# Performance work log

Measured on AMD Instinct MI355X. Metric: run time of the kernel, lower is better.

Reference implementation:

```python
import jax, jax.numpy as jnp
import numpy as np
from jax import lax

K = 9  # propagation kernel

def conv(x, w, b, pad):
    y = lax.conv_general_dilated(x, w, (1, 1), [(pad, pad), (pad, pad)],
                                 dimension_numbers=('NCHW', 'OIHW', 'NCHW'))
    return y + b[None, :, None, None]

def bn(x, g, beta):
    # SynchronizedBatchNorm2d in eval mode with identity running stats (mean=0, var=1)
    return x * g[None, :, None, None] + beta[None, :, None, None]

def propagate(deep, wts):
    # Dynamic local filtering (same math as img2col * weights, sum over 81 taps),
    # computed as 81 shifted-slice FMAs instead of materializing the (n,c,hw,81) tensor.
    p = K // 2
    n, c, h, w = deep.shape
    padded = jnp.pad(deep, ((0, 0), (0, 0), (p, p), (p, p)))
    out = jnp.zeros_like(deep)
    for k in range(K * K):  # k = dy*9 + dx, matching unfold(2).unfold(3) flattening
        dy, dx = k // K, k % K
        out = out + padded[:, :, dy:dy + h, dx:dx + w] * wts[:, k:k + 1]
    return out

def setup_inputs():
    key = jax.random.key(0)
    ks = jax.random.split(key, 40)
    N, C, H, W = 1, 256, 96, 192
    NUM_CLASSES = 19
    s = 0.05
    f32 = jnp.float32
    d = {}
    d['f1_deep'] = jax.random.normal(ks[0], (N, C, H, W), f32)
    d['f1_low'] = jax.random.normal(ks[1], (N, C, H, W), f32)
    d['f2_low'] = jax.random.normal(ks[2], (N, C, H, W), f32)
    # WeightPredictor
    d['wp_c1_w'] = jax.random.normal(ks[3], (256, 256, 3, 3), f32) * s
    d['wp_c1_b'] = jnp.zeros((256,), f32)
    d['wp_c2_w'] = jax.random.normal(ks[4], (256, 512, 3, 3), f32) * s
    d['wp_c2_b'] = jnp.zeros((256,), f32)
    d['wp_fc_w'] = jax.random.normal(ks[5], (81, 256, 1, 1), f32) * s
    d['wp_fc_b'] = jnp.zeros((81,), f32)
    # AdaptiveScheduler
    d['sch_c1_w'] = jax.random.normal(ks[6], (256, 256, 3, 3), f32) * s
    d['sch_c1_b'] = jnp.zeros((256,), f32)
    d['sch_c2_w'] = jax.random.normal(ks[7], (256, 256, 3, 3), f32) * s
    d['sch_c2_b'] = jnp.zeros((256,), f32)
    d['sch_fc_w'] = jax.random.normal(ks[8], (1, 256), f32) * s
    d['sch_fc_b'] = jnp.zeros((1,), f32)
    # AdaptNet
    d['ad_c1_w'] = jax.random.normal(ks[9], (256, 512, 3, 3), f32) * s
    d['ad_c1_b'] = jnp.zeros((256,), f32)
    d['ad_c2_w'] = jax.random.normal(ks[10], (256, 256, 3, 3), f32) * s
    d['ad_c2_b'] = jnp.zeros((256,), f32)
    d['ad_c3_w'] = jax.random.normal(ks[11], (256, 256, 3, 3), f32) * s
    d['ad_c3_b'] = jnp.zeros((256,), f32)
    # reduce_conv2 (1x1 conv + BN)
    d['rc_w'] = jax.random.normal(ks[12], (48, 256, 1, 1), f32) * s
    d['rc_b'] = jnp.zeros((48,), f32)
    d['rc_g'] = jnp.ones((48,), f32)
    d['rc_beta'] = jnp.zeros((48,), f32)
    # last_conv
    d['lc1_w'] = jax.random.normal(ks[13], (256, 304, 3, 3), f32) * s
    d['lc1_b'] = jnp.zeros((256,), f32)
    d['lc1_g'] = jnp.ones((256,), f32)
    d['lc1_beta'] = jnp.zeros((256,), f32)
    d['lc2_w'] = jax.random.normal(ks[14], (256, 256, 3, 3), f32) * s
    d['lc2_b'] = jnp.zeros((256,), f32)
    d['lc2_g'] = jnp.ones((256,), f32)
    d['lc2_beta'] = jnp.zeros((256,), f32)
    d['lc3_w'] = jax.random.normal(ks[15], (NUM_CLASSES, 256, 1, 1), f32) * s
    d['lc3_b'] = jnp.zeros((NUM_CLASSES,), f32)
    return d

def reference(f1_deep, f1_low, f2_low,
              wp_c1_w, wp_c1_b, wp_c2_w, wp_c2_b, wp_fc_w, wp_fc_b,
              sch_c1_w, sch_c1_b, sch_c2_w, sch_c2_b, sch_fc_w, sch_fc_b,
              ad_c1_w, ad_c1_b, ad_c2_w, ad_c2_b, ad_c3_w, ad_c3_b,
              rc_w, rc_b, rc_g, rc_beta,
              lc1_w, lc1_b, lc1_g, lc1_beta,
              lc2_w, lc2_b, lc2_g, lc2_beta,
              lc3_w, lc3_b):
    n, c, h, w = f1_deep.shape
    # WeightPredictor: shared conv1 applied to both low features, cat, conv2, 1x1, softmax over 81 taps
    a1 = conv(f1_low, wp_c1_w, wp_c1_b, 1)
    a2 = conv(f2_low, wp_c1_w, wp_c1_b, 1)
    f = conv(jnp.concatenate([a1, a2], axis=1), wp_c2_w, wp_c2_b, 1)
    kernel = jax.nn.softmax(conv(f, wp_fc_w, wp_fc_b, 0), axis=1)  # (n,81,h,w)
    # AdaptiveScheduler
    diff = conv(f1_low, sch_c1_w, sch_c1_b, 1) - conv(f2_low, sch_c1_w, sch_c1_b, 1)
    o = conv(diff, sch_c2_w, sch_c2_b, 1)
    pooled = jnp.mean(o, axis=(2, 3)).squeeze()  # (256,) since n=1
    deviation = pooled @ sch_fc_w.T + sch_fc_b  # (1,)
    # PropagationModule (dynamic 9x9 local filtering of f1_deep by predicted per-pixel kernel)
    prop = propagate(f1_deep, kernel)  # (n,256,h,w)
    # AdaptNet
    x = conv(jnp.concatenate([f2_low, prop], axis=1), ad_c1_w, ad_c1_b, 1)
    x = conv(x, ad_c2_w, ad_c2_b, 1)
    x = conv(x, ad_c3_w, ad_c3_b, 1)
    # reduce_conv2 + last_conv
    low = bn(conv(f2_low, rc_w, rc_b, 0), rc_g, rc_beta)  # (n,48,h,w)
    x = jnp.concatenate([x, low], axis=1)  # (n,304,h,w)
    x = bn(conv(x, lc1_w, lc1_b, 1), lc1_g, lc1_beta)
    x = bn(conv(x, lc2_w, lc2_b, 1), lc2_g, lc2_beta)
    x = conv(x, lc3_w, lc3_b, 0)  # (n,19,h,w)
    out = jax.image.resize(x, (x.shape[0], x.shape[1], 4 * h, 4 * w), method='bilinear')
    return (out, deviation)
```

## Files before the change

kernel.cpp:

```cpp
#include <hip/hip_runtime.h>
#include <math.h>

#define HWIMG 18432
#define W2 194
#define H2 98
#define NPX1 (H2 * W2)
#define W4 200
#define H4 104
#define NPX4 (H4 * W4)
#define NOUT (19 * 384 * 768)

typedef short bf16x8 __attribute__((ext_vector_type(8)));
typedef float f32x16 __attribute__((ext_vector_type(16)));

__device__ __forceinline__ ushort bf16r(float f) {
    union { float f; unsigned u; } a; a.f = f;
    unsigned u = a.u;
    return (ushort)((u + 0x7fffu + ((u >> 16) & 1u)) >> 16);
}
__device__ __forceinline__ float b2f(ushort u) {
    union { unsigned i; float f; } a; a.i = ((unsigned)u) << 16;
    return a.f;
}
__device__ __forceinline__ bf16x8 ld8(const ushort* p) {
    return *reinterpret_cast<const bf16x8*>(p);
}

__device__ __forceinline__ void gld16(const ushort* g, ushort* l) {
    __builtin_amdgcn_global_load_lds(
        (const __attribute__((address_space(1))) unsigned int*)g,
        (__attribute__((address_space(3))) unsigned int*)l, 16, 0, 0);
}

#define MF32(a, b, c) __builtin_amdgcn_mfma_f32_32x32x16_bf16(a, b, c, 0, 0, 0)


__global__ __launch_bounds__(256) void xform_t_k(const float* __restrict__ src,
                                                 const float* __restrict__ src2,
                                                 ushort* __restrict__ dst)
{
    const int px = blockIdx.x * 32 + (threadIdx.x & 31);
    const int c8 = (blockIdx.y * 8 + (threadIdx.x >> 5)) * 8;
    if (px >= NPX1) return;
    const int yP = px / W2, xP = px % W2;
    const int y = yP - 1, x = xP - 1;
    ushort v[8];
    if (y >= 0 && y < 96 && x >= 0 && x < 192) {
        const int p = y * 192 + x;
#pragma unroll
        for (int j = 0; j < 8; ++j) {
            float f = src[(size_t)(c8 + j) * HWIMG + p];
            if (src2) f -= src2[(size_t)(c8 + j) * HWIMG + p];
            v[j] = bf16r(f);
        }
    } else {
#pragma unroll
        for (int j = 0; j < 8; ++j) v[j] = 0;
    }
    *reinterpret_cast<uint4*>(dst + ((size_t)(c8 >> 4) * NPX1 + px) * 16 + (c8 & 15))
        = *reinterpret_cast<uint4*>(v);
}

__global__ __launch_bounds__(256) void xform_nhwc_k(const float* __restrict__ src,
                                                    ushort* __restrict__ dst)
{
    const int px = blockIdx.x * 8 + (threadIdx.x >> 5);
    const int c8 = (threadIdx.x & 31) * 8;
    if (px >= NPX4) return;
    const int yP = px / W4, xP = px % W4;
    const int y = yP - 4, x = xP - 4;
    ushort v[8];
    if (y >= 0 && y < 96 && x >= 0 && x < 192) {
        const int p = y * 192 + x;
#pragma unroll
        for (int j = 0; j < 8; ++j) v[j] = bf16r(src[(size_t)(c8 + j) * HWIMG + p]);
    } else {
#pragma unroll
        for (int j = 0; j < 8; ++j) v[j] = 0;
    }
    *reinterpret_cast<uint4*>(dst + (size_t)px * 256 + c8) = *reinterpret_cast<uint4*>(v);
}

__global__ __launch_bounds__(256) void borderzero3_k(ushort* __restrict__ b0,
                                                     ushort* __restrict__ b1,
                                                     ushort* __restrict__ b2)
{
    ushort* buf = (blockIdx.y == 0) ? b0 : ((blockIdx.y == 1) ? b1 : b2);
    const int idx = blockIdx.x * 256 + threadIdx.x;
    if (idx >= 580 * 16) return;
    const int pi = idx % 580;
    const int cb = idx / 580;
    int pp;
    if (pi < 194) pp = pi;
    else if (pi < 388) pp = 97 * 194 + (pi - 194);
    else if (pi < 484) pp = (pi - 388 + 1) * 194;
    else pp = (pi - 484 + 1) * 194 + 193;
    uint4 z = {0, 0, 0, 0};
    ushort* p = buf + ((size_t)cb * NPX1 + pp) * 16;
    *reinterpret_cast<uint4*>(p) = z;
    *reinterpret_cast<uint4*>(p + 8) = z;
}

struct WtxJob {
    const float* w; const float* b; const float* g; const float* beta;
    int CoutR, Coutp, CinR0, kb0e, CinR1, KBt, ntaps, wtoff, biasoff;
};

__global__ __launch_bounds__(256) void wtx_multi_k(WtxJob J0, WtxJob J1, WtxJob J2,
                                                   WtxJob J3, WtxJob J4, WtxJob J5,
                                                   ushort* __restrict__ wt,
                                                   float* __restrict__ biasout)
{
    WtxJob J = J0;
    switch (blockIdx.y) {
        case 1: J = J1; break; case 2: J = J2; break; case 3: J = J3; break;
        case 4: J = J4; break; case 5: J = J5; break; default: break;
    }
    const int idx = blockIdx.x * 256 + threadIdx.x;
    const int total = J.ntaps * J.KBt * J.Coutp * 16;
    const int CinT = J.CinR0 + J.CinR1;
    if (idx < total) {
        const int c16 = idx & 15;
        const int oc = (idx >> 4) % J.Coutp;
        const int r2 = idx / (16 * J.Coutp);
        const int tap = r2 % J.ntaps;
        const int kbt = r2 / J.ntaps;
        const int k = kbt * 16 + c16;
        float val = 0.f;
        if (oc < J.CoutR) {
            int cit = -1;
            if (k < J.kb0e) { if (k < J.CinR0) cit = k; }
            else { const int k1 = k - J.kb0e; if (k1 < J.CinR1) cit = J.CinR0 + k1; }
            if (cit >= 0) {
                val = J.w[((size_t)oc * CinT + cit) * J.ntaps + tap];
                if (J.g) val *= J.g[oc];
            }
        }
        wt[J.wtoff + idx] = bf16r(val);
    } else if (idx < total + J.Coutp) {
        const int oc = idx - total;
        float v = 0.f;
        if (oc < J.CoutR) {
            v = J.b ? J.b[oc] : 0.f;
            if (J.g) v = v * J.g[oc] + J.beta[oc];
        }
        biasout[J.biasoff + oc] = v;
    }
}

struct ConvJob {
    const ushort* in0; const ushort* in1;
    int KB0, KB1;
    const ushort* wt;
    const float* bias;
    ushort* out;
    int CoutWr;
};

template<int NTAPS>
__device__ __forceinline__ void stage_kb(
    const ConvJob& J, int kb, char* Ab, char* Bb,
    int y0, int x0, int ocb0, int Coutp, int tid)
{
    constexpr int AROWS = (NTAPS == 9) ? 4 : 2;
    constexpr int AW = (NTAPS == 9) ? 66 : 64;
    constexpr int ASLOTS = AROWS * AW * 2;
    const ushort* plane = (kb < J.KB0)
        ? (J.in0 + (size_t)kb * (NPX1 * 16))
        : (J.in1 + (size_t)(kb - J.KB0) * (NPX1 * 16));
#pragma unroll
    for (int i = 0; i < (ASLOTS + 127) / 128; ++i) {
        const int f16 = i * 128 + tid;
        if ((ASLOTS % 128 == 0) || (f16 < ASLOTS)) {
            const int e = f16 >> 1;
            const int h8 = (f16 & 1) * 8;
            const int r = e / AW;
            const int xx = e - r * AW;
            const int px = (NTAPS == 9)
                ? (y0 - 1 + r) * W2 + (x0 - 1 + xx)
                : (y0 + r) * W2 + (x0 + xx);
            gld16(plane + (size_t)px * 16 + h8,
                  (ushort*)(Ab + __builtin_amdgcn_readfirstlane((f16 & ~63) * 16)));
        }
    }
    const ushort* wsrc = J.wt + ((size_t)(kb * NTAPS) * Coutp + ocb0 + (tid >> 1)) * 16
                       + (tid & 1) * 8;
    const int wu = __builtin_amdgcn_readfirstlane((tid & ~63) * 16);
#pragma unroll
    for (int t = 0; t < NTAPS; ++t) {
        gld16(wsrc + (size_t)t * Coutp * 16, (ushort*)(Bb + t * 2048 + wu));
    }
}

template<int NTAPS>
__device__ __forceinline__ void compute_step(
    f32x16& c00, f32x16& c01, f32x16& c10, f32x16& c11,
    const char* Ab, const char* Bb, int wm, int l31, int h16)
{
    constexpr int AW = (NTAPS == 9) ? 66 : 64;
#pragma unroll
    for (int t = 0; t < NTAPS; ++t) {
        const int rowb = (NTAPS == 9) ? ((wm + t / 3) * AW + (t % 3)) : (wm * AW);
        const char* Bp = Bb + t * 2048;
        bf16x8 a0 = ld8((const ushort*)(Ab + (rowb + l31) * 32 + h16));
        bf16x8 a1 = ld8((const ushort*)(Ab + (rowb + 32 + l31) * 32 + h16));
        bf16x8 b0 = ld8((const ushort*)(Bp + l31 * 32 + h16));
        bf16x8 b1 = ld8((const ushort*)(Bp + (32 + l31) * 32 + h16));
        c00 = MF32(a0, b0, c00);
        c01 = MF32(a0, b1, c01);
        c10 = MF32(a1, b0, c10);
        c11 = MF32(a1, b1, c11);
    }
}

template<int NTAPS>
__global__ __launch_bounds__(128) void conv_lds_k(ConvJob j0, ConvJob j1, ConvJob j2,
                                                  int Coutp)
{
    constexpr int AROWS = (NTAPS == 9) ? 4 : 2;
    constexpr int AW = (NTAPS == 9) ? 66 : 64;
    constexpr int APLANE = AROWS * AW * 32;
    __shared__ __align__(128) char A0[APLANE];
    __shared__ __align__(128) char A1[APLANE];
    __shared__ __align__(128) char B0[NTAPS * 2048];
    __shared__ __align__(128) char B1[NTAPS * 2048];

    ConvJob J = j0;
    if (blockIdx.y == 1) J = j1;
    else if (blockIdx.y == 2) J = j2;

    const int nblk = gridDim.x;
    const int cpx = nblk >> 3;
    const int sw = ((int)blockIdx.x & 7) * cpx + ((int)blockIdx.x >> 3);
    const int pt = sw % 144;
    const int ocb0 = (sw / 144) * 64;
    const int y0 = (pt / 3) * 2 + 1;
    const int x0 = (pt % 3) * 64 + 1;

    const int tid = threadIdx.x;
    const int lane = tid & 63;
    const int wm = tid >> 6;
    const int l31 = lane & 31;
    const int h16 = (lane >> 5) * 16;

    const int KBtot = J.KB0 + J.KB1;

    f32x16 c00 = {}, c01 = {}, c10 = {}, c11 = {};

    stage_kb<NTAPS>(J, 0, A0, B0, y0, x0, ocb0, Coutp, tid);
    __syncthreads();

    for (int s = 0; s < KBtot; s += 2) {
        stage_kb<NTAPS>(J, s + 1, A1, B1, y0, x0, ocb0, Coutp, tid);
        __builtin_amdgcn_sched_barrier(0);
        compute_step<NTAPS>(c00, c01, c10, c11, A0, B0, wm, l31, h16);
        __syncthreads();
        if (s + 2 < KBtot)
            stage_kb<NTAPS>(J, s + 2, A0, B0, y0, x0, ocb0, Coutp, tid);
        __builtin_amdgcn_sched_barrier(0);
        compute_step<NTAPS>(c00, c01, c10, c11, A1, B1, wm, l31, h16);
        __syncthreads();
    }

    const int pxbase = (y0 + wm) * W2 + x0;
    const int rlo = (lane >> 5) * 4;
#pragma unroll
    for (int j = 0; j < 2; ++j) {
        if (ocb0 + j * 32 + 32 > J.CoutWr) continue;
        const int oc = ocb0 + j * 32 + l31;
        const float bs = J.bias[oc];
        const size_t obase = (size_t)(oc >> 4) * ((size_t)NPX1 * 16) + (oc & 15);
        const f32x16 v0 = j ? c01 : c00;
        const f32x16 v1 = j ? c11 : c10;
#pragma unroll
        for (int r = 0; r < 16; ++r) {
            const int rw = (r & 3) + 8 * (r >> 2) + rlo;
            J.out[obase + (size_t)(pxbase + rw) * 16] = bf16r(v0[r] + bs);
            J.out[obase + (size_t)(pxbase + 32 + rw) * 16] = bf16r(v1[r] + bs);
        }
    }
}

__global__ __launch_bounds__(256) void softmax81_k(ushort* __restrict__ t)
{
    const int p = blockIdx.x * 256 + threadIdx.x;
    if (p >= HWIMG) return;
    const int y = p / 192, x = p % 192;
    const size_t pp = (size_t)(y + 1) * W2 + (x + 1);
    float v[81];
    float m = -1e30f;
#pragma unroll
    for (int k = 0; k < 81; ++k) {
        v[k] = b2f(t[((size_t)(k >> 4) * NPX1 + pp) * 16 + (k & 15)]);
        m = fmaxf(m, v[k]);
    }
    float s = 0.f;
#pragma unroll
    for (int k = 0; k < 81; ++k) { v[k] = __expf(v[k] - m); s += v[k]; }
    const float inv = 1.f / s;
#pragma unroll
    for (int k = 0; k < 81; ++k)
        t[((size_t)(k >> 4) * NPX1 + pp) * 16 + (k & 15)] = bf16r(v[k] * inv);
}

__global__ __launch_bounds__(256) void prop_k(const ushort* __restrict__ deep,
                                              const ushort* __restrict__ ker,
                                              ushort* __restrict__ out)
{
    __shared__ float kl[8][81];
    const int pxb = blockIdx.x * 8;
    const int t = threadIdx.x;
    for (int i = t; i < 8 * 81; i += 256) {
        const int pp = pxb + i / 81, k = i % 81;
        float kv = 0.f;
        if (pp < NPX1) {
            const int yP = pp / W2, xP = pp % W2;
            if (yP >= 1 && yP <= 96 && xP >= 1 && xP <= 192)
                kv = b2f(ker[((size_t)(k >> 4) * NPX1 + pp) * 16 + (k & 15)]);
        }
        kl[i / 81][k] = kv;
    }
    __syncthreads();
    const int pi = t >> 5;
    const int c8 = (t & 31) * 8;
    const int pp = pxb + pi;
    if (pp >= NPX1) return;
    const int yP = pp / W2, xP = pp % W2;
    ushort* op = out + ((size_t)(c8 >> 4) * NPX1 + pp) * 16 + (c8 & 15);
    if (yP < 1 || yP > 96 || xP < 1 || xP > 192) {
        uint4 z = {0, 0, 0, 0};
        *reinterpret_cast<uint4*>(op) = z;
        return;
    }
    const int y = yP - 1, x = xP - 1;
    float acc[8];
#pragma unroll
    for (int j = 0; j < 8; ++j) acc[j] = 0.f;
    const ushort* dbase = deep + ((size_t)(y + 4) * W4 + (x + 4)) * 256 + c8;
#pragma unroll
    for (int k = 0; k < 81; ++k) {
        const int dy = k / 9 - 4, dx = k % 9 - 4;
        const float kv = kl[pi][k];
        bf16x8 d = ld8(dbase + (ptrdiff_t)(dy * W4 + dx) * 256);
#pragma unroll
        for (int j = 0; j < 8; ++j) acc[j] += b2f((ushort)d[j]) * kv;
    }
    ushort v[8];
#pragma unroll
    for (int j = 0; j < 8; ++j) v[j] = bf16r(acc[j]);
    *reinterpret_cast<uint4*>(op) = *reinterpret_cast<uint4*>(v);
}

__global__ __launch_bounds__(256) void rowsum_k(const ushort* __restrict__ t,
                                                float* __restrict__ partial)
{
    const int y = blockIdx.x >> 2;
    const int bx = blockIdx.x & 3;
    const int c = threadIdx.x;
    const size_t base = ((size_t)(c >> 4) * NPX1 + (size_t)(y + 1) * W2 + 1 + bx * 48) * 16
                      + (c & 15);
    float s = 0.f;
    for (int x = 0; x < 48; ++x) s += b2f(t[base + (size_t)x * 16]);
    partial[(size_t)blockIdx.x * 256 + c] = s;
}

__global__ __launch_bounds__(256) void dev_k(const float* __restrict__ partial,
                                             const float* __restrict__ fcw,
                                             const float* __restrict__ fcb,
                                             float* __restrict__ o)
{
    __shared__ float buf[256];
    const int c = threadIdx.x;
    float s = 0.f;
    for (int i = 0; i < 384; ++i) s += partial[(size_t)i * 256 + c];
    buf[c] = s * fcw[c];
    __syncthreads();
    for (int st = 128; st > 0; st >>= 1) {
        if (c < st) buf[c] += buf[c + st];
        __syncthreads();
    }
    if (c == 0) o[0] = buf[0] * (1.f / (float)HWIMG) + fcb[0];
}

__global__ __launch_bounds__(256) void upsample_k(const ushort* __restrict__ in,
                                                  float* __restrict__ outp)
{
    const int idx = blockIdx.x * 256 + threadIdx.x;
    if (idx >= NOUT) return;
    const int ox = idx % 768;
    const int t = idx / 768;
    const int oy = t % 384;
    const int c = t / 384;

    const float fx = (ox + 0.5f) * 0.25f - 0.5f;
    const float fy = (oy + 0.5f) * 0.25f - 0.5f;
    const int x0 = (int)floorf(fx);
    const int y0 = (int)floorf(fy);
    const float wx = fx - (float)x0;
    const float wy = fy - (float)y0;
    const int x0c = min(max(x0, 0), 191), x1c = min(max(x0 + 1, 0), 191);
    const int y0c = min(max(y0, 0), 95), y1c = min(max(y0 + 1, 0), 95);

    const size_t cb = (size_t)(c >> 4) * NPX1;
    const int c16 = c & 15;
    const float v00 = b2f(in[(cb + (size_t)(y0c + 1) * W2 + (x0c + 1)) * 16 + c16]);
    const float v01 = b2f(in[(cb + (size_t)(y0c + 1) * W2 + (x1c + 1)) * 16 + c16]);
    const float v10 = b2f(in[(cb + (size_t)(y1c + 1) * W2 + (x0c + 1)) * 16 + c16]);
    const float v11 = b2f(in[(cb + (size_t)(y1c + 1) * W2 + (x1c + 1)) * 16 + c16]);
    outp[idx] = (1.f - wy) * ((1.f - wx) * v00 + wx * v01)
              + wy * ((1.f - wx) * v10 + wx * v11);
}

extern "C" void kernel_launch(void* const* d_in, const int* in_sizes, int n_in,
                              void* d_out, int out_size, void* d_ws, size_t ws_size,
                              hipStream_t stream)
{
    const float* f1_deep = (const float*)d_in[0];
    const float* f1_low  = (const float*)d_in[1];
    const float* f2_low  = (const float*)d_in[2];
    const float* wp_c1_w = (const float*)d_in[3];
    const float* wp_c1_b = (const float*)d_in[4];
    const float* wp_c2_w = (const float*)d_in[5];
    const float* wp_c2_b = (const float*)d_in[6];
    const float* wp_fc_w = (const float*)d_in[7];
    const float* wp_fc_b = (const float*)d_in[8];
    const float* sch_c1_w = (const float*)d_in[9];
    const float* sch_c2_w = (const float*)d_in[11];
    const float* sch_c2_b = (const float*)d_in[12];
    const float* sch_fc_w = (const float*)d_in[13];
    const float* sch_fc_b = (const float*)d_in[14];
    const float* ad_c1_w = (const float*)d_in[15];
    const float* ad_c1_b = (const float*)d_in[16];
    const float* ad_c2_w = (const float*)d_in[17];
    const float* ad_c2_b = (const float*)d_in[18];
    const float* ad_c3_w = (const float*)d_in[19];
    const float* ad_c3_b = (const float*)d_in[20];
    const float* rc_w    = (const float*)d_in[21];
    const float* rc_b    = (const float*)d_in[22];
    const float* rc_g    = (const float*)d_in[23];
    const float* rc_beta = (const float*)d_in[24];
    const float* lc1_w   = (const float*)d_in[25];
    const float* lc1_b   = (const float*)d_in[26];
    const float* lc1_g   = (const float*)d_in[27];
    const float* lc1_beta= (const float*)d_in[28];
    const float* lc2_w   = (const float*)d_in[29];
    const float* lc2_b   = (const float*)d_in[30];
    const float* lc2_g   = (const float*)d_in[31];
    const float* lc2_beta= (const float*)d_in[32];
    const float* lc3_w   = (const float*)d_in[33];
    const float* lc3_b   = (const float*)d_in[34];

    float* out = (float*)d_out;
    ushort* ws0 = (ushort*)d_ws;

    const size_t CBBe  = (size_t)NPX1 * 256;
    const size_t BUF0e = (size_t)NPX4 * 256;

    ushort* Bb = ws0 + BUF0e;
    ushort* Cb = Bb + CBBe;
    ushort* Db = Cb + CBBe;
    ushort* Eb = Db + CBBe;
    ushort* Fb = Eb + CBBe;
    ushort* WT = Fb + CBBe;
    float* BIAS = (float*)(WT + 3719168);
    float* PART = (float*)ws0;
    ushort* L48 = Eb + 6 * (size_t)NPX1 * 16;

    const dim3 b256(256), b128(128);

    xform_t_k<<<dim3(595, 4), b256, 0, stream>>>(f1_low, nullptr, Bb);
    xform_t_k<<<dim3(595, 4), b256, 0, stream>>>(f2_low, nullptr, Cb);
    xform_t_k<<<dim3(595, 4), b256, 0, stream>>>(f1_low, f2_low, Db);
    borderzero3_k<<<dim3(37, 3), b256, 0, stream>>>(ws0, Eb, Fb);

    {
        WtxJob w0 = {wp_c1_w, wp_c1_b, nullptr, nullptr, 256, 256, 256, 256, 0, 16, 9, 0, 0};
        WtxJob w1 = {sch_c1_w, nullptr, nullptr, nullptr, 256, 256, 256, 256, 0, 16, 9, 589824, 256};
        WtxJob w2 = {wp_c2_w, wp_c2_b, nullptr, nullptr, 256, 256, 256, 256, 256, 32, 9, 1179648, 512};
        WtxJob w3 = {sch_c2_w, sch_c2_b, nullptr, nullptr, 256, 256, 256, 256, 0, 16, 9, 2359296, 768};
        WtxJob w4 = {wp_fc_w, wp_fc_b, nullptr, nullptr, 81, 128, 256, 256, 0, 16, 1, 2949120, 1024};
        WtxJob w5 = {rc_w, rc_b, rc_g, rc_beta, 48, 128, 256, 256, 0, 16, 1, 2981888, 1280};
        wtx_multi_k<<<dim3(4610, 6), b256, 0, stream>>>(w0, w1, w2, w3, w4, w5, WT, BIAS);
    }

    {
        ConvJob a0 = {Bb, Bb, 16, 0, WT, BIAS, Eb, 256};
        ConvJob a1 = {Cb, Cb, 16, 0, WT, BIAS, Fb, 256};
        ConvJob a2 = {Db, Db, 16, 0, WT + 589824, BIAS + 256, ws0, 256};
        conv_lds_k<9><<<dim3(576, 3), b128, 0, stream>>>(a0, a1, a2, 256);
    }
    {
        ConvJob a0 = {Eb, Fb, 16, 16, WT + 1179648, BIAS + 512, Db, 256};
        ConvJob a1 = {ws0, ws0, 16, 0, WT + 2359296, BIAS + 768, Bb, 256};
        conv_lds_k<9><<<dim3(576, 2), b128, 0, stream>>>(a0, a1, a0, 256);
    }
    rowsum_k<<<384, b256, 0, stream>>>(Bb, PART);
    dev_k<<<1, b256, 0, stream>>>(PART, sch_fc_w, sch_fc_b, out + NOUT);

    {
        ConvJob a0 = {Db, Db, 16, 0, WT + 2949120, BIAS + 1024, Eb, 96};
        ConvJob a1 = {Cb, Cb, 16, 0, WT + 2981888, BIAS + 1280, L48, 64};
        conv_lds_k<1><<<dim3(288, 2), b128, 0, stream>>>(a0, a1, a0, 128);
    }

    {
        WtxJob w0 = {ad_c1_w, ad_c1_b, nullptr, nullptr, 256, 256, 256, 256, 256, 32, 9, 0, 1536};
        WtxJob w1 = {ad_c2_w, ad_c2_b, nullptr, nullptr, 256, 256, 256, 256, 0, 16, 9, 1179648, 1792};
        WtxJob w2 = {ad_c3_w, ad_c3_b, nullptr, nullptr, 256, 256, 256, 256, 0, 16, 9, 1769472, 2048};
        WtxJob w3 = {lc1_w, lc1_b, lc1_g, lc1_beta, 256, 256, 256, 256, 48, 20, 9, 2359296, 2304};
        WtxJob w4 = {lc2_w, lc2_b, lc2_g, lc2_beta, 256, 256, 256, 256, 0, 16, 9, 3096576, 2560};
        WtxJob w5 = {lc3_w, lc3_b, nullptr, nullptr, 19, 128, 256, 256, 0, 16, 1, 3686400, 2816};
        wtx_multi_k<<<dim3(4610, 6), b256, 0, stream>>>(w0, w1, w2, w3, w4, w5, WT, BIAS);
    }

    softmax81_k<<<72, b256, 0, stream>>>(Eb);
    xform_nhwc_k<<<2600, b256, 0, stream>>>(f1_deep, ws0);
    prop_k<<<2377, b256, 0, stream>>>(ws0, Eb, Fb);

    {
        ConvJob a = {Cb, Fb, 16, 16, WT, BIAS + 1536, Bb, 256};
        conv_lds_k<9><<<dim3(576, 1), b128, 0, stream>>>(a, a, a, 256);
    }
    {
        ConvJob a = {Bb, Bb, 16, 0, WT + 1179648, BIAS + 1792, Db, 256};
        conv_lds_k<9><<<dim3(576, 1), b128, 0, stream>>>(a, a, a, 256);
    }
    {
        ConvJob a = {Db, Db, 16, 0, WT + 1769472, BIAS + 2048, Fb, 256};
        conv_lds_k<9><<<dim3(576, 1), b128, 0, stream>>>(a, a, a, 256);
    }
    {
        ConvJob a = {Fb, L48, 16, 4, WT + 2359296, BIAS + 2304, Bb, 256};
        conv_lds_k<9><<<dim3(576, 1), b128, 0, stream>>>(a, a, a, 256);
    }
    {
        ConvJob a = {Bb, Bb, 16, 0, WT + 3096576, BIAS + 2560, Db, 256};
        conv_lds_k<9><<<dim3(576, 1), b128, 0, stream>>>(a, a, a, 256);
    }
    {
        ConvJob a = {Db, Db, 16, 0, WT + 3686400, BIAS + 2816, Cb, 32};
        conv_lds_k<1><<<dim3(288, 1), b128, 0, stream>>>(a, a, a, 128);
    }

    upsample_k<<<(NOUT + 255) / 256, b256, 0, stream>>>(Cb, out);
}
```

Before: 489.6 us.

## Load conv activations directly from global memory and swizzle weight LDS layout

The conv kernel stops staging the activation halo tile into LDS and instead reads each tap's A fragments straight from global memory (relying on cache reuse across the 9 taps). The weight tile stays double-buffered in LDS but now uses an XOR swizzle to avoid bank conflicts. This removes LDS traffic and some barrier-covered staging for A, at the risk of exposed global-load latency in the MFMA loop since A is no longer prefetched.

```diff
diff --git a/kernel.cpp b/kernel.cpp
--- a/kernel.cpp
+++ b/kernel.cpp
@@ -33,6 +33,8 @@
 }
 
 #define MF32(a, b, c) __builtin_amdgcn_mfma_f32_32x32x16_bf16(a, b, c, 0, 0, 0)
+
+__device__ __forceinline__ int swz(int L) { return L ^ (((L >> 7) & 7) << 4); }
 
 
 __global__ __launch_bounds__(256) void xform_t_k(const float* __restrict__ src,
@@ -158,54 +160,38 @@
 };
 
 template<int NTAPS>
-__device__ __forceinline__ void stage_kb(
-    const ConvJob& J, int kb, char* Ab, char* Bb,
-    int y0, int x0, int ocb0, int Coutp, int tid)
-{
-    constexpr int AROWS = (NTAPS == 9) ? 4 : 2;
-    constexpr int AW = (NTAPS == 9) ? 66 : 64;
-    constexpr int ASLOTS = AROWS * AW * 2;
+__device__ __forceinline__ void stage_B(
+    const ConvJob& J, int kb, char* Bb,
+    int ocb0, int Coutp, int tid, int b_r, int b_h8, int wu)
+{
+    const ushort* wsrc = J.wt + ((size_t)(kb * NTAPS) * Coutp + ocb0 + b_r) * 16 + b_h8;
+#pragma unroll
+    for (int t = 0; t < NTAPS; ++t) {
+        gld16(wsrc + (size_t)t * Coutp * 16, (ushort*)(Bb + t * 2048 + wu));
+    }
+}
+
+template<int NTAPS>
+__device__ __forceinline__ void compute_step(
+    const ConvJob& J, int kb,
+    f32x16& c00, f32x16& c01, f32x16& c10, f32x16& c11,
+    const char* Bb, int pxbase, int lane)
+{
+    const int l31 = lane & 63 & 31;
+    const int h16 = ((lane & 63) >> 5) * 16;
     const ushort* plane = (kb < J.KB0)
         ? (J.in0 + (size_t)kb * (NPX1 * 16))
         : (J.in1 + (size_t)(kb - J.KB0) * (NPX1 * 16));
-#pragma unroll
-    for (int i = 0; i < (ASLOTS + 127) / 128; ++i) {
-        const int f16 = i * 128 + tid;
-        if ((ASLOTS % 128 == 0) || (f16 < ASLOTS)) {
-            const int e = f16 >> 1;
-            const int h8 = (f16 & 1) * 8;
-            const int r = e / AW;
-            const int xx = e - r * AW;
-            const int px = (NTAPS == 9)
-                ? (y0 - 1 + r) * W2 + (x0 - 1 + xx)
-                : (y0 + r) * W2 + (x0 + xx);
-            gld16(plane + (size_t)px * 16 + h8,
-                  (ushort*)(Ab + __builtin_amdgcn_readfirstlane((f16 & ~63) * 16)));
-        }
-    }
-    const ushort* wsrc = J.wt + ((size_t)(kb * NTAPS) * Coutp + ocb0 + (tid >> 1)) * 16
-                       + (tid & 1) * 8;
-    const int wu = __builtin_amdgcn_readfirstlane((tid & ~63) * 16);
+    const ushort* ap = plane + (size_t)(pxbase + l31) * 16 + (h16 >> 1);
 #pragma unroll
     for (int t = 0; t < NTAPS; ++t) {
-        gld16(wsrc + (size_t)t * Coutp * 16, (ushort*)(Bb + t * 2048 + wu));
-    }
-}
-
-template<int NTAPS>
-__device__ __forceinline__ void compute_step(
-    f32x16& c00, f32x16& c01, f32x16& c10, f32x16& c11,
-    const char* Ab, const char* Bb, int wm, int l31, int h16)
-{
-    constexpr int AW = (NTAPS == 9) ? 66 : 64;
-#pragma unroll
-    for (int t = 0; t < NTAPS; ++t) {
-        const int rowb = (NTAPS == 9) ? ((wm + t / 3) * AW + (t % 3)) : (wm * AW);
+        const ptrdiff_t sh = (NTAPS == 9)
+            ? (ptrdiff_t)((t / 3 - 1) * W2 + (t % 3 - 1)) * 16 : 0;
+        bf16x8 a0 = ld8(ap + sh);
+        bf16x8 a1 = ld8(ap + sh + 512);
         const char* Bp = Bb + t * 2048;
-        bf16x8 a0 = ld8((const ushort*)(Ab + (rowb + l31) * 32 + h16));
-        bf16x8 a1 = ld8((const ushort*)(Ab + (rowb + 32 + l31) * 32 + h16));
-        bf16x8 b0 = ld8((const ushort*)(Bp + l31 * 32 + h16));
-        bf16x8 b1 = ld8((const ushort*)(Bp + (32 + l31) * 32 + h16));
+        bf16x8 b0 = ld8((const ushort*)(Bp + swz(l31 * 32 + h16)));
+        bf16x8 b1 = ld8((const ushort*)(Bp + swz((32 + l31) * 32 + h16)));
         c00 = MF32(a0, b0, c00);
         c01 = MF32(a0, b1, c01);
         c10 = MF32(a1, b0, c10);
@@ -217,11 +203,6 @@
 __global__ __launch_bounds__(128) void conv_lds_k(ConvJob j0, ConvJob j1, ConvJob j2,
                                                   int Coutp)
 {
-    constexpr int AROWS = (NTAPS == 9) ? 4 : 2;
-    constexpr int AW = (NTAPS == 9) ? 66 : 64;
-    constexpr int APLANE = AROWS * AW * 32;
-    __shared__ __align__(128) char A0[APLANE];
-    __shared__ __align__(128) char A1[APLANE];
     __shared__ __align__(128) char B0[NTAPS * 2048];
     __shared__ __align__(128) char B1[NTAPS * 2048];
 
@@ -241,28 +222,32 @@
     const int lane = tid & 63;
     const int wm = tid >> 6;
     const int l31 = lane & 31;
-    const int h16 = (lane >> 5) * 16;
+    const int pxbase = (y0 + wm) * W2 + x0;
+
+    const int bl = swz(tid * 16);
+    const int b_r = bl >> 5;
+    const int b_h8 = ((bl >> 4) & 1) * 8;
+    const int wu = __builtin_amdgcn_readfirstlane((tid & ~63) * 16);
 
     const int KBtot = J.KB0 + J.KB1;
 
     f32x16 c00 = {}, c01 = {}, c10 = {}, c11 = {};
 
-    stage_kb<NTAPS>(J, 0, A0, B0, y0, x0, ocb0, Coutp, tid);
+    stage_B<NTAPS>(J, 0, B0, ocb0, Coutp, tid, b_r, b_h8, wu);
     __syncthreads();
 
     for (int s = 0; s < KBtot; s += 2) {
-        stage_kb<NTAPS>(J, s + 1, A1, B1, y0, x0, ocb0, Coutp, tid);
+        stage_B<NTAPS>(J, s + 1, B1, ocb0, Coutp, tid, b_r, b_h8, wu);
         __builtin_amdgcn_sched_barrier(0);
-        compute_step<NTAPS>(c00, c01, c10, c11, A0, B0, wm, l31, h16);
+        compute_step<NTAPS>(J, s, c00, c01, c10, c11, B0, pxbase, lane);
         __syncthreads();
         if (s + 2 < KBtot)
-            stage_kb<NTAPS>(J, s + 2, A0, B0, y0, x0, ocb0, Coutp, tid);
+            stage_B<NTAPS>(J, s + 2, B0, ocb0, Coutp, tid, b_r, b_h8, wu);
         __builtin_amdgcn_sched_barrier(0);
-        compute_step<NTAPS>(c00, c01, c10, c11, A1, B1, wm, l31, h16);
+        compute_step<NTAPS>(J, s + 1, c00, c01, c10, c11, B1, pxbase, lane);
         __syncthreads();
     }
 
-    const int pxbase = (y0 + wm) * W2 + x0;
     const int rlo = (lane >> 5) * 4;
 #pragma unroll
     for (int j = 0; j < 2; ++j) {
```

New measurement: 644.8 us. 31.7% more time.
